# Kernel optimization log

Hardware: AMD Instinct MI355X
Metric: run time of the kernel (lower is better)

Reference implementation:

```python
import jax, jax.numpy as jnp
import numpy as np

EPS = 0.0  # torch code divides by norms directly (no eps); inputs are randn so norms > 0


def setup_inputs() -> dict:
    key = jax.random.key(0)
    ks = jax.random.split(key, 16)
    B, C, H, W = 16, 64, 128, 128
    DIM = 4 * C  # 256
    f32 = jnp.float32
    inp = {
        "low": jax.random.normal(ks[0], (B, C, H, W), f32),
        "high": jax.random.normal(ks[1], (B, C, H, W), f32),
        "flow": jax.random.normal(ks[2], (B, C, H, W), f32),
        "feedback": jax.random.normal(ks[3], (B, C, H, W), f32),
        # GCN(4, 64, 64): single graph-conv layer, relu(adj @ x @ W + b)
        "Wgcn": jax.random.normal(ks[4], (C, C), f32) * 0.05,
        "bgcn": jnp.zeros((C,), f32),
        # four SE fc heads: Linear(DIM -> C) + sigmoid
        "W1": jax.random.normal(ks[5], (C, DIM), f32) * 0.05,
        "b1": jnp.zeros((C,), f32),
        "W2": jax.random.normal(ks[6], (C, DIM), f32) * 0.05,
        "b2": jnp.zeros((C,), f32),
        "W3": jax.random.normal(ks[7], (C, DIM), f32) * 0.05,
        "b3": jnp.zeros((C,), f32),
        "W4": jax.random.normal(ks[8], (C, DIM), f32) * 0.05,
        "b4": jnp.zeros((C,), f32),
        # gate: 1x1 Conv2d(DIM -> 64) stored as dense [64, DIM]
        "Wgate": jax.random.normal(ks[9], (C, DIM), f32) * 0.05,
        "bgate": jnp.zeros((C,), f32),
    }
    return inp


def reference(low, high, flow, feedback, Wgcn, bgcn, W1, b1, W2, b2, W3, b3, W4, b4, Wgate, bgate):
    B, C, H, W = low.shape
    # adaptive avg pool(1) of concat([low,high,flow,feedback], dim=1) then view(B,4,C)
    combined_fc = jnp.stack([
        low.mean(axis=(2, 3)),
        high.mean(axis=(2, 3)),
        flow.mean(axis=(2, 3)),
        feedback.mean(axis=(2, 3)),
    ], axis=1)  # [B, 4, C]
    # cosine-similarity adjacency  [B, 4, 4]
    norm = jnp.linalg.norm(combined_fc, axis=2, keepdims=True)  # [B,4,1]
    mul = jnp.einsum('bic,bjc->bij', combined_fc, combined_fc)
    batch_adj = mul / (norm * norm.transpose(0, 2, 1))
    # tiny GCN: relu(adj @ x @ W + b)  -> feat_cat = flatten over nodes
    h = jax.nn.relu(jnp.einsum('bij,bjc,cd->bid', batch_adj, combined_fc, Wgcn) + bgcn)  # [B,4,C]
    feat_cat = h.reshape(B, 4 * C)  # [B, 256]
    sig = jax.nn.sigmoid
    e1 = sig(feat_cat @ W1.T + b1)[:, :, None, None]  # [B,C,1,1]
    e2 = sig(feat_cat @ W2.T + b2)[:, :, None, None]
    e3 = sig(feat_cat @ W3.T + b3)[:, :, None, None]
    e4 = sig(feat_cat @ W4.T + b4)[:, :, None, None]
    wa = low + e2 * high + e3 * flow + e4 * feedback
    wb = e1 * low + high + e3 * flow + e4 * feedback
    wc = e1 * low + e2 * high + flow + e4 * feedback
    wd = e1 * low + e2 * high + e3 * flow + feedback
    feat = jnp.concatenate([wa, wb, wc, wd], axis=1)  # [B, 4C, H, W]
    # 1x1 conv == channel GEMM
    out = jnp.einsum('bchw,oc->bohw', feat, Wgate) + bgate[None, :, None, None]
    return out
```

## Files before the change

### kernel.cpp

```cpp
#include <hip/hip_runtime.h>
#include <cmath>

#define BB 16
#define CC 64
#define PP 16384
#define DIMF 256

__global__ __launch_bounds__(256) void k_means(const float* __restrict__ low,
                                               const float* __restrict__ high,
                                               const float* __restrict__ flow,
                                               const float* __restrict__ fb,
                                               float* __restrict__ cf) {
    int bc = blockIdx.x;
    int b = bc >> 6, c = bc & 63;
    int tid = threadIdx.x;
    size_t base = (size_t)bc * PP;
    const float* in[4] = {low, high, flow, fb};
    __shared__ float red[256];
    for (int t = 0; t < 4; ++t) {
        const float4* p = (const float4*)(in[t] + base);
        float s = 0.f;
        #pragma unroll 4
        for (int i = tid; i < PP / 4; i += 256) {
            float4 v = p[i];
            s += (v.x + v.y) + (v.z + v.w);
        }
        red[tid] = s;
        __syncthreads();
        for (int off = 128; off > 0; off >>= 1) {
            if (tid < off) red[tid] += red[tid + off];
            __syncthreads();
        }
        if (tid == 0) cf[(b * 4 + t) * CC + c] = red[0] * (1.0f / PP);
        __syncthreads();
    }
}

__global__ __launch_bounds__(256) void k_small(const float* __restrict__ cf,
    const float* __restrict__ Wgcn, const float* __restrict__ bgcn,
    const float* __restrict__ W1, const float* __restrict__ b1,
    const float* __restrict__ W2, const float* __restrict__ b2,
    const float* __restrict__ W3, const float* __restrict__ b3,
    const float* __restrict__ W4, const float* __restrict__ b4,
    const float* __restrict__ Wgate,
    float* __restrict__ Amat) {
    int b = blockIdx.x;
    int tid = threadIdx.x;
    __shared__ float x[4][64];
    __shared__ float nrm[4];
    __shared__ float adj[16];
    __shared__ float y[4][64];
    __shared__ float fc[256];
    __shared__ float e[4][64];

    x[tid >> 6][tid & 63] = cf[b * 256 + tid];
    __syncthreads();

    if (tid < 4) {
        float s = 0.f;
        for (int c = 0; c < 64; ++c) s += x[tid][c] * x[tid][c];
        nrm[tid] = sqrtf(s);
    }
    __syncthreads();

    if (tid < 16) {
        int i = tid >> 2, j = tid & 3;
        float s = 0.f;
        for (int c = 0; c < 64; ++c) s += x[i][c] * x[j][c];
        adj[tid] = s / (nrm[i] * nrm[j]);
    }
    __syncthreads();

    {
        int i = tid >> 6, c = tid & 63;
        float s = 0.f;
        for (int j = 0; j < 4; ++j) s += adj[i * 4 + j] * x[j][c];
        y[i][c] = s;
    }
    __syncthreads();

    {
        int i = tid >> 6, d = tid & 63;
        float s = bgcn[d];
        for (int c = 0; c < 64; ++c) s += y[i][c] * Wgcn[c * 64 + d];
        fc[i * 64 + d] = fmaxf(s, 0.f);
    }
    __syncthreads();

    {
        int k = tid >> 6, c = tid & 63;
        const float* Wk = (k == 0) ? W1 : (k == 1) ? W2 : (k == 2) ? W3 : W4;
        const float* bk = (k == 0) ? b1 : (k == 1) ? b2 : (k == 2) ? b3 : b4;
        float s = bk[c];
        for (int d = 0; d < 256; ++d) s += fc[d] * Wk[c * 256 + d];
        e[k][c] = 1.f / (1.f + expf(-s));
    }
    __syncthreads();

    float* Ab = Amat + b * 4 * 64 * 64;
    for (int ii = tid; ii < 4 * 64 * 64; ii += 256) {
        int t = ii >> 12, c = (ii >> 6) & 63, o = ii & 63;
        float w0 = Wgate[o * 256 + 0   + c];
        float w1 = Wgate[o * 256 + 64  + c];
        float w2 = Wgate[o * 256 + 128 + c];
        float w3 = Wgate[o * 256 + 192 + c];
        float wt = (t == 0) ? w0 : (t == 1) ? w1 : (t == 2) ? w2 : w3;
        float sum = (w0 + w1) + (w2 + w3);
        Ab[ii] = wt + e[t][c] * (sum - wt);
    }
}

__global__ __launch_bounds__(256) void k_gemm(const float* __restrict__ low,
    const float* __restrict__ high, const float* __restrict__ flow,
    const float* __restrict__ fb, const float* __restrict__ Amat,
    const float* __restrict__ bgate, float* __restrict__ out) {
    int blk = blockIdx.x;
    int b = blk >> 6;
    int tile = blk & 63;
    int tid = threadIdx.x;
    int pt = tid & 63;
    int og = __builtin_amdgcn_readfirstlane(tid >> 6);
    int p0 = tile * 256 + pt * 4;

    const float* in[4] = {low, high, flow, fb};
    float acc[16][4];
    #pragma unroll
    for (int j = 0; j < 16; ++j)
        #pragma unroll
        for (int q = 0; q < 4; ++q) acc[j][q] = 0.f;

    const float* Ab = Amat + b * 16384 + og * 16;
    #pragma unroll 1
    for (int t = 0; t < 4; ++t) {
        const float* xp = in[t] + (size_t)b * CC * PP + p0;
        const float* Ap = Ab + t * 4096;
        #pragma unroll 2
        for (int c = 0; c < 64; ++c) {
            float4 xv = *(const float4*)(xp + (size_t)c * PP);
            const float* Ar = Ap + c * 64;
            #pragma unroll
            for (int j = 0; j < 16; ++j) {
                float a = Ar[j];
                acc[j][0] = fmaf(a, xv.x, acc[j][0]);
                acc[j][1] = fmaf(a, xv.y, acc[j][1]);
                acc[j][2] = fmaf(a, xv.z, acc[j][2]);
                acc[j][3] = fmaf(a, xv.w, acc[j][3]);
            }
        }
    }

    #pragma unroll
    for (int j = 0; j < 16; ++j) {
        int o = og * 16 + j;
        float bg = bgate[o];
        float4 r = make_float4(acc[j][0] + bg, acc[j][1] + bg,
                               acc[j][2] + bg, acc[j][3] + bg);
        *(float4*)(out + ((size_t)(b * CC + o)) * PP + p0) = r;
    }
}

extern "C" void kernel_launch(void* const* d_in, const int* in_sizes, int n_in,
                              void* d_out, int out_size, void* d_ws, size_t ws_size,
                              hipStream_t stream) {
    const float* low  = (const float*)d_in[0];
    const float* high = (const float*)d_in[1];
    const float* flow = (const float*)d_in[2];
    const float* fb   = (const float*)d_in[3];
    const float* Wgcn = (const float*)d_in[4];
    const float* bgcn = (const float*)d_in[5];
    const float* W1   = (const float*)d_in[6];
    const float* b1   = (const float*)d_in[7];
    const float* W2   = (const float*)d_in[8];
    const float* b2   = (const float*)d_in[9];
    const float* W3   = (const float*)d_in[10];
    const float* b3   = (const float*)d_in[11];
    const float* W4   = (const float*)d_in[12];
    const float* b4   = (const float*)d_in[13];
    const float* Wgate = (const float*)d_in[14];
    const float* bgate = (const float*)d_in[15];
    float* out = (float*)d_out;

    float* cf   = (float*)d_ws;
    float* Amat = (float*)d_ws + 4096;

    k_means<<<BB * CC, 256, 0, stream>>>(low, high, flow, fb, cf);
    k_small<<<BB, 256, 0, stream>>>(cf, Wgcn, bgcn, W1, b1, W2, b2, W3, b3,
                                    W4, b4, Wgate, Amat);
    k_gemm<<<BB * CC, 256, 0, stream>>>(low, high, flow, fb, Amat, bgate, out);
}
```

Before: 431.2 us.

## Split mean reduction per tensor, interleave GEMM inputs, vectorize small kernel, nontemporal stores

The means kernel now launches one block per (batch, tensor, channel) and reduces with wave shuffles instead of a shared-memory tree, giving more parallelism and fewer barriers. The small kernel computes the SE heads with vectorized loads plus wave reductions, and builds the folded gate matrix with vectorized weight reads. The GEMM kernel loads all four input tensors in each channel iteration instead of looping over tensors, adds an occupancy hint to launch bounds, and writes output with nontemporal stores. The interleaved loads raise register pressure and may cause spills under the occupancy hint.

```diff
diff --git a/kernel.cpp b/kernel.cpp
--- a/kernel.cpp
+++ b/kernel.cpp
@@ -4,36 +4,34 @@
 #define BB 16
 #define CC 64
 #define PP 16384
-#define DIMF 256
+
+typedef float f32x4 __attribute__((ext_vector_type(4)));
 
 __global__ __launch_bounds__(256) void k_means(const float* __restrict__ low,
                                                const float* __restrict__ high,
                                                const float* __restrict__ flow,
                                                const float* __restrict__ fb,
                                                float* __restrict__ cf) {
-    int bc = blockIdx.x;
-    int b = bc >> 6, c = bc & 63;
+    int blk = blockIdx.x;
+    int b = blk >> 8, t = (blk >> 6) & 3, c = blk & 63;
+    const float* in = (t == 0) ? low : (t == 1) ? high : (t == 2) ? flow : fb;
+    const float4* p = (const float4*)(in + ((size_t)(b * CC + c)) * PP);
     int tid = threadIdx.x;
-    size_t base = (size_t)bc * PP;
-    const float* in[4] = {low, high, flow, fb};
-    __shared__ float red[256];
-    for (int t = 0; t < 4; ++t) {
-        const float4* p = (const float4*)(in[t] + base);
-        float s = 0.f;
-        #pragma unroll 4
-        for (int i = tid; i < PP / 4; i += 256) {
-            float4 v = p[i];
-            s += (v.x + v.y) + (v.z + v.w);
-        }
-        red[tid] = s;
-        __syncthreads();
-        for (int off = 128; off > 0; off >>= 1) {
-            if (tid < off) red[tid] += red[tid + off];
-            __syncthreads();
-        }
-        if (tid == 0) cf[(b * 4 + t) * CC + c] = red[0] * (1.0f / PP);
-        __syncthreads();
-    }
+
+    float s = 0.f;
+    #pragma unroll
+    for (int i = 0; i < 16; ++i) {
+        float4 v = p[tid + i * 256];
+        s += (v.x + v.y) + (v.z + v.w);
+    }
+    #pragma unroll
+    for (int off = 32; off > 0; off >>= 1) s += __shfl_down(s, off, 64);
+
+    __shared__ float r[4];
+    if ((tid & 63) == 0) r[tid >> 6] = s;
+    __syncthreads();
+    if (tid == 0)
+        cf[(b * 4 + t) * CC + c] = ((r[0] + r[1]) + (r[2] + r[3])) * (1.0f / PP);
 }
 
 __global__ __launch_bounds__(256) void k_small(const float* __restrict__ cf,
@@ -46,6 +44,8 @@
     float* __restrict__ Amat) {
     int b = blockIdx.x;
     int tid = threadIdx.x;
+    int lane = tid & 63;
+    int wid = tid >> 6;
     __shared__ float x[4][64];
     __shared__ float nrm[4];
     __shared__ float adj[16];
@@ -53,7 +53,7 @@
     __shared__ float fc[256];
     __shared__ float e[4][64];
 
-    x[tid >> 6][tid & 63] = cf[b * 256 + tid];
+    x[wid][lane] = cf[b * 256 + tid];
     __syncthreads();
 
     if (tid < 4) {
@@ -72,45 +72,62 @@
     __syncthreads();
 
     {
-        int i = tid >> 6, c = tid & 63;
         float s = 0.f;
-        for (int j = 0; j < 4; ++j) s += adj[i * 4 + j] * x[j][c];
-        y[i][c] = s;
-    }
-    __syncthreads();
-
-    {
-        int i = tid >> 6, d = tid & 63;
-        float s = bgcn[d];
-        for (int c = 0; c < 64; ++c) s += y[i][c] * Wgcn[c * 64 + d];
-        fc[i * 64 + d] = fmaxf(s, 0.f);
-    }
-    __syncthreads();
-
-    {
-        int k = tid >> 6, c = tid & 63;
-        const float* Wk = (k == 0) ? W1 : (k == 1) ? W2 : (k == 2) ? W3 : W4;
-        const float* bk = (k == 0) ? b1 : (k == 1) ? b2 : (k == 2) ? b3 : b4;
-        float s = bk[c];
-        for (int d = 0; d < 256; ++d) s += fc[d] * Wk[c * 256 + d];
-        e[k][c] = 1.f / (1.f + expf(-s));
-    }
-    __syncthreads();
-
-    float* Ab = Amat + b * 4 * 64 * 64;
-    for (int ii = tid; ii < 4 * 64 * 64; ii += 256) {
-        int t = ii >> 12, c = (ii >> 6) & 63, o = ii & 63;
-        float w0 = Wgate[o * 256 + 0   + c];
-        float w1 = Wgate[o * 256 + 64  + c];
-        float w2 = Wgate[o * 256 + 128 + c];
-        float w3 = Wgate[o * 256 + 192 + c];
-        float wt = (t == 0) ? w0 : (t == 1) ? w1 : (t == 2) ? w2 : w3;
-        float sum = (w0 + w1) + (w2 + w3);
-        Ab[ii] = wt + e[t][c] * (sum - wt);
-    }
-}
-
-__global__ __launch_bounds__(256) void k_gemm(const float* __restrict__ low,
+        #pragma unroll
+        for (int j = 0; j < 4; ++j) s += adj[wid * 4 + j] * x[j][lane];
+        y[wid][lane] = s;
+    }
+    __syncthreads();
+
+    {
+        float s = bgcn[lane];
+        for (int c = 0; c < 64; ++c) s += y[wid][c] * Wgcn[c * 64 + lane];
+        fc[wid * 64 + lane] = fmaxf(s, 0.f);
+    }
+    __syncthreads();
+
+    {
+        const float* Wk = (wid == 0) ? W1 : (wid == 1) ? W2 : (wid == 2) ? W3 : W4;
+        const float* bk = (wid == 0) ? b1 : (wid == 1) ? b2 : (wid == 2) ? b3 : b4;
+        float4 fv = *(const float4*)&fc[lane * 4];
+        for (int c = 0; c < 64; ++c) {
+            float4 w = *(const float4*)(Wk + c * 256 + lane * 4);
+            float part = (w.x * fv.x + w.y * fv.y) + (w.z * fv.z + w.w * fv.w);
+            #pragma unroll
+            for (int off = 32; off > 0; off >>= 1)
+                part += __shfl_down(part, off, 64);
+            if (lane == 0) {
+                float s = part + bk[c];
+                e[wid][c] = 1.f / (1.f + expf(-s));
+            }
+        }
+    }
+    __syncthreads();
+
+    {
+        int t = wid, o = lane;
+        const float* wrow = Wgate + o * 256;
+        float* Ab = Amat + b * 16384 + t * 4096;
+        #pragma unroll 4
+        for (int c4 = 0; c4 < 64; c4 += 4) {
+            float4 w0 = *(const float4*)(wrow + c4);
+            float4 w1 = *(const float4*)(wrow + 64 + c4);
+            float4 w2 = *(const float4*)(wrow + 128 + c4);
+            float4 w3 = *(const float4*)(wrow + 192 + c4);
+            float4 wt = (t == 0) ? w0 : (t == 1) ? w1 : (t == 2) ? w2 : w3;
+            float4 sm = make_float4((w0.x + w1.x) + (w2.x + w3.x),
+                                    (w0.y + w1.y) + (w2.y + w3.y),
+                                    (w0.z + w1.z) + (w2.z + w3.z),
+                                    (w0.w + w1.w) + (w2.w + w3.w));
+            Ab[(c4 + 0) * 64 + o] = wt.x + e[t][c4 + 0] * (sm.x - wt.x);
+            Ab[(c4 + 1) * 64 + o] = wt.y + e[t][c4 + 1] * (sm.y - wt.y);
+            Ab[(c4 + 2) * 64 + o] = wt.z + e[t][c4 + 2] * (sm.z - wt.z);
+            Ab[(c4 + 3) * 64 + o] = wt.w + e[t][c4 + 3] * (sm.w - wt.w);
+        }
+    }
+}
+
+__global__ __launch_bounds__(256, 4) void k_gemm(const float* __restrict__ low,
     const float* __restrict__ high, const float* __restrict__ flow,
     const float* __restrict__ fb, const float* __restrict__ Amat,
     const float* __restrict__ bgate, float* __restrict__ out) {
@@ -122,30 +139,36 @@
     int og = __builtin_amdgcn_readfirstlane(tid >> 6);
     int p0 = tile * 256 + pt * 4;
 
-    const float* in[4] = {low, high, flow, fb};
+    size_t xoff = (size_t)b * (CC * PP) + p0;
+    const float* pl = low  + xoff;
+    const float* ph = high + xoff;
+    const float* pf = flow + xoff;
+    const float* pb = fb   + xoff;
+    const float* Ab = Amat + b * 16384 + og * 16;
+
     float acc[16][4];
     #pragma unroll
     for (int j = 0; j < 16; ++j)
         #pragma unroll
         for (int q = 0; q < 4; ++q) acc[j][q] = 0.f;
 
-    const float* Ab = Amat + b * 16384 + og * 16;
-    #pragma unroll 1
-    for (int t = 0; t < 4; ++t) {
-        const float* xp = in[t] + (size_t)b * CC * PP + p0;
-        const float* Ap = Ab + t * 4096;
-        #pragma unroll 2
-        for (int c = 0; c < 64; ++c) {
-            float4 xv = *(const float4*)(xp + (size_t)c * PP);
-            const float* Ar = Ap + c * 64;
-            #pragma unroll
-            for (int j = 0; j < 16; ++j) {
-                float a = Ar[j];
-                acc[j][0] = fmaf(a, xv.x, acc[j][0]);
-                acc[j][1] = fmaf(a, xv.y, acc[j][1]);
-                acc[j][2] = fmaf(a, xv.z, acc[j][2]);
-                acc[j][3] = fmaf(a, xv.w, acc[j][3]);
-            }
+    #pragma unroll 2
+    for (int c = 0; c < 64; ++c) {
+        float4 x0 = *(const float4*)(pl + (size_t)c * PP);
+        float4 x1 = *(const float4*)(ph + (size_t)c * PP);
+        float4 x2 = *(const float4*)(pf + (size_t)c * PP);
+        float4 x3 = *(const float4*)(pb + (size_t)c * PP);
+        const float* A0 = Ab + c * 64;
+        #pragma unroll
+        for (int j = 0; j < 16; ++j) {
+            float a0 = A0[j];
+            float a1 = A0[4096 + j];
+            float a2 = A0[8192 + j];
+            float a3 = A0[12288 + j];
+            acc[j][0] += a0 * x0.x + a1 * x1.x + a2 * x2.x + a3 * x3.x;
+            acc[j][1] += a0 * x0.y + a1 * x1.y + a2 * x2.y + a3 * x3.y;
+            acc[j][2] += a0 * x0.z + a1 * x1.z + a2 * x2.z + a3 * x3.z;
+            acc[j][3] += a0 * x0.w + a1 * x1.w + a2 * x2.w + a3 * x3.w;
         }
     }
 
@@ -153,9 +176,10 @@
     for (int j = 0; j < 16; ++j) {
         int o = og * 16 + j;
         float bg = bgate[o];
-        float4 r = make_float4(acc[j][0] + bg, acc[j][1] + bg,
-                               acc[j][2] + bg, acc[j][3] + bg);
-        *(float4*)(out + ((size_t)(b * CC + o)) * PP + p0) = r;
+        f32x4 r;
+        r.x = acc[j][0] + bg; r.y = acc[j][1] + bg;
+        r.z = acc[j][2] + bg; r.w = acc[j][3] + bg;
+        __builtin_nontemporal_store(r, (f32x4*)(out + ((size_t)(b * CC + o)) * PP + p0));
     }
 }
 
@@ -183,7 +207,7 @@
     float* cf   = (float*)d_ws;
     float* Amat = (float*)d_ws + 4096;
 
-    k_means<<<BB * CC, 256, 0, stream>>>(low, high, flow, fb, cf);
+    k_means<<<BB * 4 * CC, 256, 0, stream>>>(low, high, flow, fb, cf);
     k_small<<<BB, 256, 0, stream>>>(cf, Wgcn, bgcn, W1, b1, W2, b2, W3, b3,
                                     W4, b4, Wgate, Amat);
     k_gemm<<<BB * CC, 256, 0, stream>>>(low, high, flow, fb, Amat, bgate, out);
```

Measured after the change: 450.5 us. 4.5% more time.
